# Kernel optimization log

Hardware: AMD Instinct MI355X
Metric: run time of the kernel (lower is better)

Reference implementation:

```python
import jax, jax.numpy as jnp
import numpy as np


def setup_inputs() -> dict:
    key = jax.random.key(0)
    inp = jax.random.normal(key, (8, 3, 224, 224), dtype=jnp.float32)
    return {"inp": inp, "tau_min": 1, "tau_max": 60, "ntau": 8,
            "num_angles": 12, "stride": 2}


def _logpolar_offsets(tau_min, tau_max, ntau, num_angles):
    # Matches the torch module: theta in [-pi, pi), tau logarithmically spaced,
    # coords stacked angle-major as (y, x) pairs (theta unsqueeze(1) outer).
    c = (tau_max / tau_min) ** (1.0 / (ntau - 1)) - 1.0
    theta = np.arange(num_angles, dtype=np.float64) * (2.0 * np.pi / num_angles) - np.pi
    tau = tau_min * (1.0 + c) ** np.arange(ntau, dtype=np.float64)
    x = tau[None, :] * np.cos(theta[:, None])   # (A, T)
    y = tau[None, :] * np.sin(theta[:, None])   # (A, T)
    return (jnp.asarray(y.ravel(), jnp.float32),
            jnp.asarray(x.ravel(), jnp.float32))  # each (A*T,)


def reference(inp, tau_min, tau_max, ntau, num_angles, stride):
    yoff, xoff = _logpolar_offsets(tau_min, tau_max, ntau, num_angles)
    B, F, H, W = inp.shape
    Hs = (H - 1) // stride + 1
    Ws = (W - 1) // stride + 1
    gy = jnp.arange(Hs, dtype=jnp.float32) * stride   # focus-point rows
    gx = jnp.arange(Ws, dtype=jnp.float32) * stride   # focus-point cols

    def sample(yo, xo):
        # Bilinear sample of inp at (i*stride + yo, j*stride + xo), zero outside.
        yq = gy + yo
        xq = gx + xo
        y0 = jnp.floor(yq)
        x0 = jnp.floor(xq)
        wy = (yq - y0)  # (Hs,)
        wx = (xq - x0)  # (Ws,)
        y0i = y0.astype(jnp.int32)
        x0i = x0.astype(jnp.int32)

        def gather(yi, xi):
            vy = ((yi >= 0) & (yi < H)).astype(inp.dtype)
            vx = ((xi >= 0) & (xi < W)).astype(inp.dtype)
            g = inp[:, :, jnp.clip(yi, 0, H - 1), :][:, :, :, jnp.clip(xi, 0, W - 1)]
            return g * (vy[:, None] * vx[None, :])  # (B,F,Hs,Ws)

        w00 = (1 - wy)[:, None] * (1 - wx)[None, :]
        w01 = (1 - wy)[:, None] * wx[None, :]
        w10 = wy[:, None] * (1 - wx)[None, :]
        w11 = wy[:, None] * wx[None, :]
        return (w00 * gather(y0i, x0i) + w01 * gather(y0i, x0i + 1)
                + w10 * gather(y0i + 1, x0i) + w11 * gather(y0i + 1, x0i + 1))

    out = jax.vmap(sample)(yoff, xoff)                    # (A*T, B, F, Hs, Ws)
    out = out.reshape(num_angles, ntau, B, F, Hs, Ws)
    out = jnp.transpose(out, (2, 3, 1, 0, 4, 5))          # (B, F, ntau, A, Hs, Ws)
    return out
```

## Files before the change

### kernel.cpp

```cpp
#include <hip/hip_runtime.h>
#include <cmath>

#ifndef M_PI
#define M_PI 3.14159265358979323846
#endif

#define B_ 8
#define F_ 3
#define H_ 224
#define W_ 224
#define T_ 8
#define A_ 12
#define NK 96
#define STRIDE_ 2
#define HS_ 112
#define WS_ 112
#define PLANE_ (H_ * W_)
#define SLICE_ (HS_ * WS_)

struct LPArgs {
    int   cx[NK];
    int   cy[NK];
    float fx[NK];
    float fy[NK];
};

static LPArgs make_args() {
    LPArgs r;
    double c = pow(60.0, 1.0 / 7.0) - 1.0;
    for (int t = 0; t < T_; ++t) {
        double tau = pow(1.0 + c, (double)t);
        for (int ang = 0; ang < A_; ++ang) {
            double theta = (double)ang * (2.0 * M_PI / (double)A_) - M_PI;
            float yo = (float)(tau * sin(theta));
            float xo = (float)(tau * cos(theta));
            int y = t * A_ + ang;
            float yf = floorf(yo), xf = floorf(xo);
            r.cy[y] = (int)yf; r.fy[y] = yo - yf;
            r.cx[y] = (int)xf; r.fx[y] = xo - xf;
        }
    }
    return r;
}

__global__ __launch_bounds__(256) void lp_sample_kernel(
    const float* __restrict__ inp, float* __restrict__ out, LPArgs args) {

    const int y  = blockIdx.y;
    const int bf = blockIdx.z;
    const int j  = threadIdx.x & 127;
    const int iband = __builtin_amdgcn_readfirstlane(threadIdx.x >> 7);

    const int   cx = args.cx[y];
    const float fx = args.fx[y];
    const int   cy = args.cy[y];
    const float fy = args.fy[y];

    int ix0 = STRIDE_ * j + cx;
    int bx  = min(max(ix0, 0), W_ - 2);
    float wA, wB;
    if (ix0 >= 0 && ix0 <= W_ - 2)  { wA = 1.0f - fx; wB = fx; }
    else if (ix0 == -1)             { wA = fx;        wB = 0.0f; }
    else if (ix0 == W_ - 1)         { wA = 0.0f;      wB = 1.0f - fx; }
    else                            { wA = 0.0f;      wB = 0.0f; }

    const float* plane = inp + (size_t)bf * PLANE_;
    const int i0 = blockIdx.x * 16 + iband;
    float* orow = out + ((size_t)bf * NK + y) * SLICE_ + (size_t)i0 * WS_ + j;

    const bool active = (j < WS_);

#pragma unroll
    for (int s = 0; s < 8; ++s) {
        int iy0 = STRIDE_ * (i0 + 2 * s) + cy;
        float mA, mB;
        if (iy0 >= 0 && iy0 <= H_ - 2)  { mA = 1.0f - fy; mB = fy; }
        else if (iy0 == -1)             { mA = fy;        mB = 0.0f; }
        else if (iy0 == H_ - 1)         { mA = 0.0f;      mB = 1.0f - fy; }
        else                            { mA = 0.0f;      mB = 0.0f; }
        int by = min(max(iy0, 0), H_ - 2);

        const float* p = plane + by * W_ + bx;
        float g0x = p[0],  g0y = p[1];
        float g1x = p[W_], g1y = p[W_ + 1];

        float h0 = wA * g0x + wB * g0y;
        float h1 = wA * g1x + wB * g1y;
        float r  = mA * h0 + mB * h1;

        if (active) orow[s * 2 * WS_] = r;
    }
}

extern "C" void kernel_launch(void* const* d_in, const int* in_sizes, int n_in,
                              void* d_out, int out_size, void* d_ws, size_t ws_size,
                              hipStream_t stream) {
    const float* inp = (const float*)d_in[0];
    float*       out = (float*)d_out;

    static const LPArgs args = make_args();

    dim3 grid(HS_ / 16, NK, B_ * F_);
    lp_sample_kernel<<<grid, 256, 0, stream>>>(inp, out, args);
}
```

Measured before the change: 158.6 us.

## Stage input row band in LDS and sample all offsets per block

```diff
diff --git a/kernel.cpp b/kernel.cpp
--- a/kernel.cpp
+++ b/kernel.cpp
@@ -18,6 +18,9 @@
 #define PLANE_ (H_ * W_)
 #define SLICE_ (HS_ * WS_)
 
+#define RI 4
+#define BAND (2 * RI + 119)
+
 struct LPArgs {
     int   cx[NK];
     int   cy[NK];
@@ -34,61 +37,80 @@
             double theta = (double)ang * (2.0 * M_PI / (double)A_) - M_PI;
             float yo = (float)(tau * sin(theta));
             float xo = (float)(tau * cos(theta));
-            int y = t * A_ + ang;
+            int k = t * A_ + ang;
             float yf = floorf(yo), xf = floorf(xo);
-            r.cy[y] = (int)yf; r.fy[y] = yo - yf;
-            r.cx[y] = (int)xf; r.fx[y] = xo - xf;
+            r.cy[k] = (int)yf; r.fy[k] = yo - yf;
+            r.cx[k] = (int)xf; r.fx[k] = xo - xf;
         }
     }
     return r;
 }
 
-__global__ __launch_bounds__(256) void lp_sample_kernel(
+__global__ __launch_bounds__(1024) void lp_sample_kernel(
     const float* __restrict__ inp, float* __restrict__ out, LPArgs args) {
 
-    const int y  = blockIdx.y;
-    const int bf = blockIdx.z;
-    const int j  = threadIdx.x & 127;
-    const int iband = __builtin_amdgcn_readfirstlane(threadIdx.x >> 7);
+    __shared__ float lds[BAND * W_];
 
-    const int   cx = args.cx[y];
-    const float fx = args.fx[y];
-    const int   cy = args.cy[y];
-    const float fy = args.fy[y];
-
-    int ix0 = STRIDE_ * j + cx;
-    int bx  = min(max(ix0, 0), W_ - 2);
-    float wA, wB;
-    if (ix0 >= 0 && ix0 <= W_ - 2)  { wA = 1.0f - fx; wB = fx; }
-    else if (ix0 == -1)             { wA = fx;        wB = 0.0f; }
-    else if (ix0 == W_ - 1)         { wA = 0.0f;      wB = 1.0f - fx; }
-    else                            { wA = 0.0f;      wB = 0.0f; }
+    const int bf  = blockIdx.x;
+    const int i0  = blockIdx.y * RI;
+    const int r0  = max(0, 2 * i0 - 60);
+    const int r1  = min(H_ - 1, 2 * i0 + 2 * RI + 58);
+    const int tid = threadIdx.x;
 
     const float* plane = inp + (size_t)bf * PLANE_;
-    const int i0 = blockIdx.x * 16 + iband;
-    float* orow = out + ((size_t)bf * NK + y) * SLICE_ + (size_t)i0 * WS_ + j;
 
-    const bool active = (j < WS_);
+    {
+        const float4* src4 = (const float4*)(plane + r0 * W_);
+        float4*       dst4 = (float4*)lds;
+        const int n4 = (r1 - r0 + 1) * (W_ / 4);
+        for (int v = tid; v < n4; v += 1024) dst4[v] = src4[v];
+    }
+    __syncthreads();
 
-#pragma unroll
-    for (int s = 0; s < 8; ++s) {
-        int iy0 = STRIDE_ * (i0 + 2 * s) + cy;
+    const int lane = tid & 63;
+    const int wave = __builtin_amdgcn_readfirstlane(tid >> 6);
+    const int di   = wave & 3;
+    const int kb   = wave >> 2;
+    const int i    = i0 + di;
+
+    float* outbase = out + (size_t)bf * NK * SLICE_ + (size_t)i * WS_;
+
+#pragma unroll 1
+    for (int n = 0; n < 24; ++n) {
+        const int k = kb + 4 * n;
+        const int   cy = args.cy[k]; const float fy = args.fy[k];
+        const int   cx = args.cx[k]; const float fx = args.fx[k];
+
+        const int iy0 = 2 * i + cy;
         float mA, mB;
         if (iy0 >= 0 && iy0 <= H_ - 2)  { mA = 1.0f - fy; mB = fy; }
         else if (iy0 == -1)             { mA = fy;        mB = 0.0f; }
         else if (iy0 == H_ - 1)         { mA = 0.0f;      mB = 1.0f - fy; }
         else                            { mA = 0.0f;      mB = 0.0f; }
-        int by = min(max(iy0, 0), H_ - 2);
+        const int by = min(max(iy0, 0), H_ - 2);
+        const float* lrow = lds + (by - r0) * W_;
 
-        const float* p = plane + by * W_ + bx;
-        float g0x = p[0],  g0y = p[1];
-        float g1x = p[W_], g1y = p[W_ + 1];
+        float* orow = outbase + (size_t)k * SLICE_;
 
-        float h0 = wA * g0x + wB * g0y;
-        float h1 = wA * g1x + wB * g1y;
-        float r  = mA * h0 + mB * h1;
+#pragma unroll
+        for (int h = 0; h < 2; ++h) {
+            const int j   = h * 64 + lane;
+            const int ix0 = 2 * j + cx;
+            float wA, wB;
+            if (ix0 >= 0 && ix0 <= W_ - 2)  { wA = 1.0f - fx; wB = fx; }
+            else if (ix0 == -1)             { wA = fx;        wB = 0.0f; }
+            else if (ix0 == W_ - 1)         { wA = 0.0f;      wB = 1.0f - fx; }
+            else                            { wA = 0.0f;      wB = 0.0f; }
+            const int bx = min(max(ix0, 0), W_ - 2);
 
-        if (active) orow[s * 2 * WS_] = r;
+            float g00 = lrow[bx],      g01 = lrow[bx + 1];
+            float g10 = lrow[W_ + bx], g11 = lrow[W_ + bx + 1];
+
+            float r = mA * (wA * g00 + wB * g01)
+                    + mB * (wA * g10 + wB * g11);
+
+            if (h == 0 || j < WS_) orow[j] = r;
+        }
     }
 }
 
@@ -100,6 +122,6 @@
 
     static const LPArgs args = make_args();
 
-    dim3 grid(HS_ / 16, NK, B_ * F_);
-    lp_sample_kernel<<<grid, 256, 0, stream>>>(inp, out, args);
+    dim3 grid(B_ * F_, HS_ / RI);
+    lp_sample_kernel<<<grid, 1024, 0, stream>>>(inp, out, args);
 }
```

After: 153.0 us. 1.04x faster.
